# Kernel optimization log

Measured on AMD Instinct MI355X. Metric: run time of the kernel, lower is better.

## Reference

```python
import jax, jax.numpy as jnp
import numpy as np

EPS = 1e-8  # torch.nn.CosineSimilarity default eps

B, N, C, H, W = 256, 5, 640, 10, 10
OC, OH, OW = 32, 5, 5  # AdaptiveAvgPool3d output (input_dim, 5, 5)


def _pool(v):
    # Adaptive avg pool over last 3 dims (C,H,W) -> (OC,OH,OW).
    # Exact block-mean since C%OC==0, H%OH==0, W%OW==0.
    lead = v.shape[:-3]
    v = v.reshape(lead + (OC, C // OC, OH, H // OH, OW, W // OW))
    return v.mean(axis=(-5, -3, -1))


def setup_inputs() -> dict:
    key = jax.random.key(0)
    x = jax.random.normal(key, (B, N, C, H, W), dtype=jnp.float32)
    return {"x": x}


def reference(x) -> jnp.ndarray:
    b, n = x.shape[0], x.shape[1]
    # proxy: pool of the sum over shots -> [B, OC*OH*OW]
    proxy = _pool(x.sum(axis=1)).reshape(b, -1)
    # per-shot pooled features -> [B, N, OC*OH*OW]
    feats = _pool(x).reshape(b, n, -1)
    # cosine similarity (torch formula: dot / max(||a||*||b||, eps))
    dot = jnp.einsum('bnd,bd->bn', feats, proxy)
    na = jnp.linalg.norm(feats, axis=-1)          # [B, N]
    nb = jnp.linalg.norm(proxy, axis=-1)[:, None]  # [B, 1]
    sim = dot / jnp.maximum(na * nb, EPS)          # [B, N]
    # weighted sum of raw shot features -> [B, C, H, W]
    out = jnp.einsum('bn,bnchw->bchw', sim, x)
    return out
```

## Files before the change

kernel.cpp:

```cpp
#include <hip/hip_runtime.h>

#define BB 256
#define NN 5
#define CHW 64000
#define DD 800
#define EPSF 1e-8f

#define NBLOCKS 128
#define TPB 1024

typedef float f4 __attribute__((ext_vector_type(4)));

__global__ __launch_bounds__(TPB) void k_fused(const float* __restrict__ x,
                                               float* __restrict__ out) {
    __shared__ float feats[NN][DD];
    __shared__ float s_sim[NN];
    const int tid = threadIdx.x;

    for (int b = blockIdx.x; b < BB; b += gridDim.x) {
        const float* __restrict__ xb = x + (size_t)b * NN * CHW;

        for (int idx = tid; idx < NN * DD; idx += TPB) {
            const int n = idx / DD;
            const int d = idx - n * DD;
            const int oc  = d / 25;
            const int rem = d - oc * 25;
            const int oh  = rem / 5;
            const int ow  = rem - oh * 5;
            const float2* __restrict__ xp =
                reinterpret_cast<const float2*>(xb + (size_t)n * CHW);
            const int base = oc * 20 * 50 + oh * 10 + ow;
            float s = 0.f;
            #pragma unroll
            for (int cc = 0; cc < 20; ++cc) {
                float2 a = xp[base + cc * 50];
                float2 c = xp[base + cc * 50 + 5];
                s += (a.x + a.y) + (c.x + c.y);
            }
            feats[n][d] = s * (1.0f / 80.0f);
        }
        __syncthreads();

        if (tid < 64) {
            float dot[NN] = {0.f, 0.f, 0.f, 0.f, 0.f};
            float na2[NN] = {0.f, 0.f, 0.f, 0.f, 0.f};
            float nb2 = 0.f;
            for (int d = tid; d < DD; d += 64) {
                float f[NN];
                float p = 0.f;
                #pragma unroll
                for (int n = 0; n < NN; ++n) { f[n] = feats[n][d]; p += f[n]; }
                #pragma unroll
                for (int n = 0; n < NN; ++n) {
                    dot[n] += f[n] * p;
                    na2[n] += f[n] * f[n];
                }
                nb2 += p * p;
            }
            #pragma unroll
            for (int off = 32; off >= 1; off >>= 1) {
                #pragma unroll
                for (int n = 0; n < NN; ++n) {
                    dot[n] += __shfl_down(dot[n], off, 64);
                    na2[n] += __shfl_down(na2[n], off, 64);
                }
                nb2 += __shfl_down(nb2, off, 64);
            }
            if (tid == 0) {
                const float nb = sqrtf(nb2);
                #pragma unroll
                for (int n = 0; n < NN; ++n) {
                    const float denom = fmaxf(sqrtf(na2[n]) * nb, EPSF);
                    s_sim[n] = dot[n] / denom;
                }
            }
        }
        __syncthreads();

        const float s0 = s_sim[0];
        const float s1 = s_sim[1];
        const float s2 = s_sim[2];
        const float s3 = s_sim[3];
        const float s4 = s_sim[4];
        const f4* __restrict__ xp4 = reinterpret_cast<const f4*>(xb);
        f4* __restrict__ op4 = reinterpret_cast<f4*>(out + (size_t)b * CHW);
        for (int i = tid; i < CHW / 4; i += TPB) {
            f4 o = s0 * xp4[i]
                 + s1 * xp4[i + 1 * (CHW / 4)]
                 + s2 * xp4[i + 2 * (CHW / 4)]
                 + s3 * xp4[i + 3 * (CHW / 4)]
                 + s4 * xp4[i + 4 * (CHW / 4)];
            __builtin_nontemporal_store(o, op4 + i);
        }
        __syncthreads();
    }
}

extern "C" void kernel_launch(void* const* d_in, const int* in_sizes, int n_in,
                              void* d_out, int out_size, void* d_ws, size_t ws_size,
                              hipStream_t stream) {
    const float* x = (const float*)d_in[0];
    float* out = (float*)d_out;
    k_fused<<<NBLOCKS, TPB, 0, stream>>>(x, out);
}
```

Measured before the change: 141.7 us.

## Launch one block per batch, vectorize pooling loads, parallelize cosine reduction

Grid changes from 128 blocks looping over batches to 256 blocks with one batch each, so all compute units get work. Pooling now uses 800 threads, each loading contiguous float4 rows and producing five outputs, which replaces strided float2 loads. The dot and norm reduction is spread across all 16 waves with a shared-memory cross-wave combine, where before a single wave did it. The cost is one more barrier, plus added register pressure from the launch-bounds occupancy hint.

Measured after the change: 129.1 us. 8.9% less time.

```diff
diff --git a/kernel.cpp b/kernel.cpp
--- a/kernel.cpp
+++ b/kernel.cpp
@@ -5,94 +5,109 @@
 #define CHW 64000
 #define DD 800
 #define EPSF 1e-8f
-
-#define NBLOCKS 128
 #define TPB 1024
 
 typedef float f4 __attribute__((ext_vector_type(4)));
 
-__global__ __launch_bounds__(TPB) void k_fused(const float* __restrict__ x,
-                                               float* __restrict__ out) {
-    __shared__ float feats[NN][DD];
+__global__ __launch_bounds__(TPB, 4) void k_fused(const float* __restrict__ x,
+                                                  float* __restrict__ out) {
+    __shared__ float feats[NN * DD];
+    __shared__ float red[17][11];
     __shared__ float s_sim[NN];
     const int tid = threadIdx.x;
+    const int b = blockIdx.x;
+    const float* __restrict__ xb = x + (size_t)b * NN * CHW;
 
-    for (int b = blockIdx.x; b < BB; b += gridDim.x) {
-        const float* __restrict__ xb = x + (size_t)b * NN * CHW;
+    if (tid < NN * 160) {
+        const int n  = tid / 160;
+        const int r  = tid - n * 160;
+        const int oc = r / 5;
+        const int oh = r - oc * 5;
+        const f4* __restrict__ p = reinterpret_cast<const f4*>(xb) +
+                                   (size_t)n * (CHW / 4) + oc * 500 + oh * 5;
+        float s0 = 0.f, s1 = 0.f, s2 = 0.f, s3 = 0.f, s4 = 0.f;
+        #pragma unroll 4
+        for (int cc = 0; cc < 20; ++cc) {
+            const f4 v0 = p[cc * 25 + 0];
+            const f4 v1 = p[cc * 25 + 1];
+            const f4 v2 = p[cc * 25 + 2];
+            const f4 v3 = p[cc * 25 + 3];
+            const f4 v4 = p[cc * 25 + 4];
+            s0 += (v0.x + v0.y) + (v2.z + v2.w);
+            s1 += (v0.z + v0.w) + (v3.x + v3.y);
+            s2 += (v1.x + v1.y) + (v3.z + v3.w);
+            s3 += (v1.z + v1.w) + (v4.x + v4.y);
+            s4 += (v2.x + v2.y) + (v4.z + v4.w);
+        }
+        float* fp = feats + n * DD + oc * 25 + oh * 5;
+        fp[0] = s0 * (1.f / 80.f);
+        fp[1] = s1 * (1.f / 80.f);
+        fp[2] = s2 * (1.f / 80.f);
+        fp[3] = s3 * (1.f / 80.f);
+        fp[4] = s4 * (1.f / 80.f);
+    }
+    __syncthreads();
 
-        for (int idx = tid; idx < NN * DD; idx += TPB) {
-            const int n = idx / DD;
-            const int d = idx - n * DD;
-            const int oc  = d / 25;
-            const int rem = d - oc * 25;
-            const int oh  = rem / 5;
-            const int ow  = rem - oh * 5;
-            const float2* __restrict__ xp =
-                reinterpret_cast<const float2*>(xb + (size_t)n * CHW);
-            const int base = oc * 20 * 50 + oh * 10 + ow;
-            float s = 0.f;
-            #pragma unroll
-            for (int cc = 0; cc < 20; ++cc) {
-                float2 a = xp[base + cc * 50];
-                float2 c = xp[base + cc * 50 + 5];
-                s += (a.x + a.y) + (c.x + c.y);
-            }
-            feats[n][d] = s * (1.0f / 80.0f);
+    float dot[NN] = {0.f, 0.f, 0.f, 0.f, 0.f};
+    float na2[NN] = {0.f, 0.f, 0.f, 0.f, 0.f};
+    float nb2 = 0.f;
+    if (tid < DD) {
+        float f[NN];
+        float pr = 0.f;
+        #pragma unroll
+        for (int n = 0; n < NN; ++n) { f[n] = feats[n * DD + tid]; pr += f[n]; }
+        #pragma unroll
+        for (int n = 0; n < NN; ++n) { dot[n] = f[n] * pr; na2[n] = f[n] * f[n]; }
+        nb2 = pr * pr;
+    }
+    #pragma unroll
+    for (int off = 32; off >= 1; off >>= 1) {
+        #pragma unroll
+        for (int n = 0; n < NN; ++n) {
+            dot[n] += __shfl_down(dot[n], off, 64);
+            na2[n] += __shfl_down(na2[n], off, 64);
         }
-        __syncthreads();
+        nb2 += __shfl_down(nb2, off, 64);
+    }
+    const int wv = tid >> 6;
+    if ((tid & 63) == 0) {
+        #pragma unroll
+        for (int n = 0; n < NN; ++n) { red[wv][n] = dot[n]; red[wv][5 + n] = na2[n]; }
+        red[wv][10] = nb2;
+    }
+    __syncthreads();
+    if (tid < 11) {
+        float s = 0.f;
+        #pragma unroll
+        for (int w = 0; w < 16; ++w) s += red[w][tid];
+        red[16][tid] = s;
+    }
+    __syncthreads();
+    if (tid == 0) {
+        const float nb = sqrtf(red[16][10]);
+        #pragma unroll
+        for (int n = 0; n < NN; ++n) {
+            const float denom = fmaxf(sqrtf(red[16][5 + n]) * nb, EPSF);
+            s_sim[n] = red[16][n] / denom;
+        }
+    }
+    __syncthreads();
 
-        if (tid < 64) {
-            float dot[NN] = {0.f, 0.f, 0.f, 0.f, 0.f};
-            float na2[NN] = {0.f, 0.f, 0.f, 0.f, 0.f};
-            float nb2 = 0.f;
-            for (int d = tid; d < DD; d += 64) {
-                float f[NN];
-                float p = 0.f;
-                #pragma unroll
-                for (int n = 0; n < NN; ++n) { f[n] = feats[n][d]; p += f[n]; }
-                #pragma unroll
-                for (int n = 0; n < NN; ++n) {
-                    dot[n] += f[n] * p;
-                    na2[n] += f[n] * f[n];
-                }
-                nb2 += p * p;
-            }
-            #pragma unroll
-            for (int off = 32; off >= 1; off >>= 1) {
-                #pragma unroll
-                for (int n = 0; n < NN; ++n) {
-                    dot[n] += __shfl_down(dot[n], off, 64);
-                    na2[n] += __shfl_down(na2[n], off, 64);
-                }
-                nb2 += __shfl_down(nb2, off, 64);
-            }
-            if (tid == 0) {
-                const float nb = sqrtf(nb2);
-                #pragma unroll
-                for (int n = 0; n < NN; ++n) {
-                    const float denom = fmaxf(sqrtf(na2[n]) * nb, EPSF);
-                    s_sim[n] = dot[n] / denom;
-                }
-            }
-        }
-        __syncthreads();
-
-        const float s0 = s_sim[0];
-        const float s1 = s_sim[1];
-        const float s2 = s_sim[2];
-        const float s3 = s_sim[3];
-        const float s4 = s_sim[4];
-        const f4* __restrict__ xp4 = reinterpret_cast<const f4*>(xb);
-        f4* __restrict__ op4 = reinterpret_cast<f4*>(out + (size_t)b * CHW);
-        for (int i = tid; i < CHW / 4; i += TPB) {
-            f4 o = s0 * xp4[i]
-                 + s1 * xp4[i + 1 * (CHW / 4)]
-                 + s2 * xp4[i + 2 * (CHW / 4)]
-                 + s3 * xp4[i + 3 * (CHW / 4)]
-                 + s4 * xp4[i + 4 * (CHW / 4)];
-            __builtin_nontemporal_store(o, op4 + i);
-        }
-        __syncthreads();
+    const float w0 = s_sim[0];
+    const float w1 = s_sim[1];
+    const float w2 = s_sim[2];
+    const float w3 = s_sim[3];
+    const float w4 = s_sim[4];
+    const f4* __restrict__ xp4 = reinterpret_cast<const f4*>(xb);
+    f4* __restrict__ op4 = reinterpret_cast<f4*>(out + (size_t)b * CHW);
+    #pragma unroll 2
+    for (int i = tid; i < CHW / 4; i += TPB) {
+        f4 o = w0 * xp4[i]
+             + w1 * xp4[i + 1 * (CHW / 4)]
+             + w2 * xp4[i + 2 * (CHW / 4)]
+             + w3 * xp4[i + 3 * (CHW / 4)]
+             + w4 * xp4[i + 4 * (CHW / 4)];
+        __builtin_nontemporal_store(o, op4 + i);
     }
 }
 
@@ -101,5 +116,5 @@
                               hipStream_t stream) {
     const float* x = (const float*)d_in[0];
     float* out = (float*)d_out;
-    k_fused<<<NBLOCKS, TPB, 0, stream>>>(x, out);
+    k_fused<<<BB, TPB, 0, stream>>>(x, out);
 }
```

## Split each batch across 8 cooperating blocks with LDS staging and global reduction

Applied to the files above, without the earlier changes.

Each batch element is now handled by 8 blocks, each owning an 80-channel slice. A block stages its slice of all 5 shots into LDS (160KB), computes partial dot and norm sums, and publishes them to a workspace. It then spins on an atomic counter until all 8 slices are done and applies the weighted sum from LDS, so x is read from HBM only once instead of twice. The grid grows to 256 blocks. The cost is a memset, a cross-block spin barrier that relies on all 256 blocks being co-resident to avoid deadlock, and heavy LDS use that limits occupancy to one block per CU.

After: 223.4 us. +57.6%, slower.

```diff
diff --git a/kernel.cpp b/kernel.cpp
--- a/kernel.cpp
+++ b/kernel.cpp
@@ -3,94 +3,126 @@
 #define BB 256
 #define NN 5
 #define CHW 64000
-#define DD 800
 #define EPSF 1e-8f
-
-#define NBLOCKS 128
 #define TPB 1024
+#define JBLK 8
+#define CHB 80
+#define CELLS 100
 
 typedef float f4 __attribute__((ext_vector_type(4)));
 
-__global__ __launch_bounds__(TPB) void k_fused(const float* __restrict__ x,
-                                               float* __restrict__ out) {
-    __shared__ float feats[NN][DD];
+__global__ __launch_bounds__(TPB, 4) void k_coop(const float* __restrict__ x,
+                                                 float* __restrict__ out,
+                                                 float* __restrict__ g_part,
+                                                 int* __restrict__ g_cnt) {
+    __shared__ float xl[NN * CHB * 100];
+    __shared__ float feats_l[CELLS][6];
+    __shared__ float red[2][11];
     __shared__ float s_sim[NN];
     const int tid = threadIdx.x;
+    const int set = blockIdx.x >> 3;
+    const int j   = blockIdx.x & 7;
 
-    for (int b = blockIdx.x; b < BB; b += gridDim.x) {
-        const float* __restrict__ xb = x + (size_t)b * NN * CHW;
+    for (int it = 0; it < BB / 32; ++it) {
+        const int b = it * 32 + set;
 
-        for (int idx = tid; idx < NN * DD; idx += TPB) {
-            const int n = idx / DD;
-            const int d = idx - n * DD;
-            const int oc  = d / 25;
-            const int rem = d - oc * 25;
-            const int oh  = rem / 5;
-            const int ow  = rem - oh * 5;
-            const float2* __restrict__ xp =
-                reinterpret_cast<const float2*>(xb + (size_t)n * CHW);
-            const int base = oc * 20 * 50 + oh * 10 + ow;
+        const f4* __restrict__ xg = reinterpret_cast<const f4*>(x);
+        #pragma unroll
+        for (int n = 0; n < NN; ++n) {
+            const f4* __restrict__ src = xg + ((size_t)(b * NN + n) * 640 + (size_t)CHB * j) * 25;
+            f4* __restrict__ dst = reinterpret_cast<f4*>(xl + n * (CHB * 100));
+            for (int i = tid; i < CHB * 25; i += TPB)
+                dst[i] = src[i];
+        }
+        __syncthreads();
+
+        if (tid < NN * CELLS) {
+            const int n    = tid / CELLS;
+            const int cell = tid - n * CELLS;
+            const int ocl  = cell / 25;
+            const int c25  = cell - ocl * 25;
+            const int oh   = c25 / 5;
+            const int ow   = c25 - oh * 5;
+            const float* __restrict__ bp =
+                xl + n * (CHB * 100) + (ocl * 20) * 100 + oh * 20 + ow * 2;
             float s = 0.f;
             #pragma unroll
             for (int cc = 0; cc < 20; ++cc) {
-                float2 a = xp[base + cc * 50];
-                float2 c = xp[base + cc * 50 + 5];
-                s += (a.x + a.y) + (c.x + c.y);
+                const float* q = bp + cc * 100;
+                s += (q[0] + q[1]) + (q[10] + q[11]);
             }
-            feats[n][d] = s * (1.0f / 80.0f);
+            feats_l[cell][n] = s * (1.f / 80.f);
         }
         __syncthreads();
 
-        if (tid < 64) {
-            float dot[NN] = {0.f, 0.f, 0.f, 0.f, 0.f};
-            float na2[NN] = {0.f, 0.f, 0.f, 0.f, 0.f};
-            float nb2 = 0.f;
-            for (int d = tid; d < DD; d += 64) {
-                float f[NN];
-                float p = 0.f;
-                #pragma unroll
-                for (int n = 0; n < NN; ++n) { f[n] = feats[n][d]; p += f[n]; }
-                #pragma unroll
-                for (int n = 0; n < NN; ++n) {
-                    dot[n] += f[n] * p;
-                    na2[n] += f[n] * f[n];
-                }
-                nb2 += p * p;
-            }
+        float part[11];
+        #pragma unroll
+        for (int k = 0; k < 11; ++k) part[k] = 0.f;
+        if (tid < CELLS) {
+            float f[NN], p = 0.f;
+            #pragma unroll
+            for (int n = 0; n < NN; ++n) { f[n] = feats_l[tid][n]; p += f[n]; }
+            #pragma unroll
+            for (int n = 0; n < NN; ++n) { part[n] = f[n] * p; part[5 + n] = f[n] * f[n]; }
+            part[10] = p * p;
+        }
+        if (tid < 128) {
             #pragma unroll
             for (int off = 32; off >= 1; off >>= 1) {
                 #pragma unroll
-                for (int n = 0; n < NN; ++n) {
-                    dot[n] += __shfl_down(dot[n], off, 64);
-                    na2[n] += __shfl_down(na2[n], off, 64);
-                }
-                nb2 += __shfl_down(nb2, off, 64);
+                for (int k = 0; k < 11; ++k)
+                    part[k] += __shfl_down(part[k], off, 64);
             }
-            if (tid == 0) {
-                const float nb = sqrtf(nb2);
+            if ((tid & 63) == 0) {
                 #pragma unroll
-                for (int n = 0; n < NN; ++n) {
-                    const float denom = fmaxf(sqrtf(na2[n]) * nb, EPSF);
-                    s_sim[n] = dot[n] / denom;
-                }
+                for (int k = 0; k < 11; ++k) red[tid >> 6][k] = part[k];
             }
         }
         __syncthreads();
 
-        const float s0 = s_sim[0];
-        const float s1 = s_sim[1];
-        const float s2 = s_sim[2];
-        const float s3 = s_sim[3];
-        const float s4 = s_sim[4];
-        const f4* __restrict__ xp4 = reinterpret_cast<const f4*>(xb);
-        f4* __restrict__ op4 = reinterpret_cast<f4*>(out + (size_t)b * CHW);
-        for (int i = tid; i < CHW / 4; i += TPB) {
-            f4 o = s0 * xp4[i]
-                 + s1 * xp4[i + 1 * (CHW / 4)]
-                 + s2 * xp4[i + 2 * (CHW / 4)]
-                 + s3 * xp4[i + 3 * (CHW / 4)]
-                 + s4 * xp4[i + 4 * (CHW / 4)];
-            __builtin_nontemporal_store(o, op4 + i);
+        if (tid == 0) {
+            #pragma unroll
+            for (int k = 0; k < 11; ++k) {
+                const float v = red[0][k] + red[1][k];
+                __hip_atomic_store(&g_part[(b * JBLK + j) * 11 + k], v,
+                                   __ATOMIC_RELAXED, __HIP_MEMORY_SCOPE_AGENT);
+            }
+            __hip_atomic_fetch_add(&g_cnt[b], 1,
+                                   __ATOMIC_RELEASE, __HIP_MEMORY_SCOPE_AGENT);
+            while (__hip_atomic_load(&g_cnt[b],
+                                     __ATOMIC_ACQUIRE, __HIP_MEMORY_SCOPE_AGENT) < JBLK)
+                __builtin_amdgcn_s_sleep(16);
+            float tot[11];
+            #pragma unroll
+            for (int k = 0; k < 11; ++k) tot[k] = 0.f;
+            for (int jj = 0; jj < JBLK; ++jj) {
+                #pragma unroll
+                for (int k = 0; k < 11; ++k)
+                    tot[k] += __hip_atomic_load(&g_part[(b * JBLK + jj) * 11 + k],
+                                                __ATOMIC_RELAXED, __HIP_MEMORY_SCOPE_AGENT);
+            }
+            const float nb = sqrtf(tot[10]);
+            #pragma unroll
+            for (int n = 0; n < NN; ++n)
+                s_sim[n] = tot[n] / fmaxf(sqrtf(tot[5 + n]) * nb, EPSF);
+        }
+        __syncthreads();
+
+        const float w0 = s_sim[0];
+        const float w1 = s_sim[1];
+        const float w2 = s_sim[2];
+        const float w3 = s_sim[3];
+        const float w4 = s_sim[4];
+        const f4* __restrict__ xl4 = reinterpret_cast<const f4*>(xl);
+        f4* __restrict__ og = reinterpret_cast<f4*>(out) +
+                              ((size_t)b * 640 + (size_t)CHB * j) * 25;
+        for (int i = tid; i < CHB * 25; i += TPB) {
+            f4 o = w0 * xl4[i]
+                 + w1 * xl4[i + 2000]
+                 + w2 * xl4[i + 4000]
+                 + w3 * xl4[i + 6000]
+                 + w4 * xl4[i + 8000];
+            __builtin_nontemporal_store(o, og + i);
         }
         __syncthreads();
     }
@@ -101,5 +133,8 @@
                               hipStream_t stream) {
     const float* x = (const float*)d_in[0];
     float* out = (float*)d_out;
-    k_fused<<<NBLOCKS, TPB, 0, stream>>>(x, out);
+    int* g_cnt = (int*)d_ws;
+    float* g_part = (float*)((char*)d_ws + 1024);
+    hipMemsetAsync(d_ws, 0, 1024 + (size_t)BB * JBLK * 11 * sizeof(float), stream);
+    k_coop<<<BB, TPB, 0, stream>>>(x, out, g_part, g_cnt);
 }
```
